# Kernel optimization log

Measured on AMD Instinct MI355X. Metric: run time of the kernel, lower is better.

Reference implementation:

```python
import jax, jax.numpy as jnp
import numpy as np

N_HEADS = 8
N_POINTS = 4
LN_EPS = 1e-5


def _ln(x, g, b):
    m = jnp.mean(x, -1, keepdims=True)
    v = jnp.mean((x - m) ** 2, -1, keepdims=True)
    return (x - m) * jax.lax.rsqrt(v + LN_EPS) * g + b


def _mha(q, k, v, wq, bq, wk, bk, wv, bv, wo, bo):
    B, Lq, C = q.shape
    Dh = C // N_HEADS
    Q = (q @ wq.T + bq).reshape(B, Lq, N_HEADS, Dh)
    K = (k @ wk.T + bk).reshape(B, -1, N_HEADS, Dh)
    V = (v @ wv.T + bv).reshape(B, -1, N_HEADS, Dh)
    s = jnp.einsum('bqhd,bkhd->bhqk', Q, K) * (1.0 / float(np.sqrt(Dh)))
    a = jax.nn.softmax(s, -1)
    o = jnp.einsum('bhqk,bkhd->bqhd', a, V).reshape(B, Lq, C)
    return o @ wo.T + bo


def _ref_points(h, w, L):
    ry = jnp.linspace(0.5, h - 0.5, h) / h
    rx = jnp.linspace(0.5, w - 0.5, w) / w
    gy, gx = jnp.meshgrid(ry, rx, indexing='ij')
    ref = jnp.stack([gx.reshape(-1), gy.reshape(-1)], -1)[None]  # (1, h*w, 2)
    return jnp.broadcast_to(ref[:, :, None, :], (1, h * w, L, 2))


def _deform_core(value, shapes, starts, loc, aw):
    # value: (B, Len_in, H, Dh); loc: (B, Lq, H, L, P, 2); aw: (B, Lq, H, L, P)
    B, _, H, Dh = value.shape
    Lq, P = loc.shape[1], loc.shape[4]
    out = jnp.zeros((B, H, Lq, Dh), value.dtype)
    for l in range(shapes.shape[0]):
        Hl, Wl = int(shapes[l, 0]), int(shapes[l, 1])
        s = int(starts[l])
        v = value[:, s:s + Hl * Wl].transpose(0, 2, 1, 3)  # (B, H, Hl*Wl, Dh)
        # grid_sample(align_corners=False, padding_mode='zeros') pixel coords
        xl = loc[:, :, :, l, :, 0] * Wl - 0.5  # (B, Lq, H, P)
        yl = loc[:, :, :, l, :, 1] * Hl - 0.5
        x0 = jnp.floor(xl); y0 = jnp.floor(yl)
        fx = xl - x0; fy = yl - y0
        x0 = x0.astype(jnp.int32); y0 = y0.astype(jnp.int32)
        acc = jnp.zeros((B, H, Lq, P, Dh), value.dtype)
        for dy, dx in ((0, 0), (0, 1), (1, 0), (1, 1)):
            xi = x0 + dx; yi = y0 + dy
            wgt = (fx if dx else 1.0 - fx) * (fy if dy else 1.0 - fy)
            valid = ((xi >= 0) & (xi < Wl) & (yi >= 0) & (yi < Hl)).astype(value.dtype)
            idx = (jnp.clip(yi, 0, Hl - 1) * Wl + jnp.clip(xi, 0, Wl - 1))
            idx = idx.transpose(0, 2, 1, 3).reshape(B, H, Lq * P)
            g = jnp.take_along_axis(v, idx[..., None], axis=2).reshape(B, H, Lq, P, Dh)
            acc = acc + g * (wgt * valid).transpose(0, 2, 1, 3)[..., None]
        out = out + jnp.einsum('bhqpd,bqhp->bhqd', acc, aw[:, :, :, l])
    return out.transpose(0, 2, 1, 3).reshape(B, Lq, H * Dh)


def reference(tgt, query_pos, src, wq, bq, wk, bk, wv, bv, wo, bo, ln2_g, ln2_b,
              w_off, b_off, w_attn, b_attn, w_val, b_val, w_cout, b_cout,
              ln1_g, ln1_b, w1, b1, w2, b2, ln3_g, ln3_b,
              src_spatial_shapes, level_start_index, h, w):
    shapes = np.asarray(src_spatial_shapes)
    starts = np.asarray(level_start_index)
    h = int(h); w = int(w)
    L = shapes.shape[0]
    B, Lq, C = tgt.shape
    Dh = C // N_HEADS
    # --- self attention (post-LN residual) ---
    q = tgt + query_pos
    t2 = _mha(q, q, tgt, wq, bq, wk, bk, wv, bv, wo, bo)
    t = _ln(tgt + t2, ln2_g, ln2_b)
    # --- MSDeformAttn cross attention ---
    qc = t + query_pos
    value = (src @ w_val.T + b_val).reshape(B, -1, N_HEADS, Dh)
    off = (qc @ w_off.T + b_off).reshape(B, Lq, N_HEADS, L, N_POINTS, 2)
    aw = (qc @ w_attn.T + b_attn).reshape(B, Lq, N_HEADS, L * N_POINTS)
    aw = jax.nn.softmax(aw, -1).reshape(B, Lq, N_HEADS, L, N_POINTS)
    norm = jnp.stack([shapes[:, 1].astype(np.float32), shapes[:, 0].astype(np.float32)], -1)  # (L,2): (W,H)
    rp = _ref_points(h, w, L)  # (1, Lq, L, 2)
    loc = rp[:, :, None, :, None, :] + off / norm[None, None, None, :, None, :]
    samp = _deform_core(value, shapes, starts, loc, aw)
    t2 = samp @ w_cout.T + b_cout
    t = _ln(t + t2, ln1_g, ln1_b)
    # --- FFN ---
    t2 = jax.nn.relu(t @ w1.T + b1) @ w2.T + b2
    t = _ln(t + t2, ln3_g, ln3_b)
    return t


def setup_inputs() -> dict:
    key = jax.random.key(0)
    B, C, L, P, dff = 2, 256, 4, 4, 1024
    h = w = 48
    shapes = np.array([[48, 48], [24, 24], [12, 12], [6, 6]], np.int32)
    starts = np.array([0, 2304, 2880, 3024], np.int32)
    Len_in = 3060
    Lq = h * w
    ks = iter(jax.random.split(key, 40))
    def rn(shape, s=0.02):
        return jax.random.normal(next(ks), shape, jnp.float32) * s
    return dict(
        tgt=rn((B, Lq, C), 1.0), query_pos=rn((B, Lq, C), 1.0), src=rn((B, Len_in, C), 1.0),
        wq=rn((C, C)), bq=rn((C,)), wk=rn((C, C)), bk=rn((C,)), wv=rn((C, C)), bv=rn((C,)),
        wo=rn((C, C)), bo=rn((C,)),
        ln2_g=jnp.ones((C,)), ln2_b=jnp.zeros((C,)),
        w_off=rn((N_HEADS * L * P * 2, C)), b_off=rn((N_HEADS * L * P * 2,)),
        w_attn=rn((N_HEADS * L * P, C)), b_attn=rn((N_HEADS * L * P,)),
        w_val=rn((C, C)), b_val=rn((C,)), w_cout=rn((C, C)), b_cout=rn((C,)),
        ln1_g=jnp.ones((C,)), ln1_b=jnp.zeros((C,)),
        w1=rn((dff, C)), b1=rn((dff,)), w2=rn((C, dff)), b2=rn((C,)),
        ln3_g=jnp.ones((C,)), ln3_b=jnp.zeros((C,)),
        src_spatial_shapes=shapes, level_start_index=starts, h=h, w=w)
```

## Files before the change

kernel.cpp:

```cpp
#include <hip/hip_runtime.h>
#include <hip/hip_bf16.h>
#include <math.h>

typedef __hip_bfloat16 bf16;
typedef __attribute__((ext_vector_type(8))) short short8;
typedef __attribute__((ext_vector_type(4))) short short4v;
typedef __attribute__((ext_vector_type(4))) float f32x4;

static constexpr int B   = 2;
static constexpr int LQ  = 2304;
static constexpr int C   = 256;
static constexpr int NH  = 8;
static constexpr int DH  = 32;
static constexpr int NL  = 4;
static constexpr int NP  = 4;
static constexpr int LEN = 3060;
static constexpr int DFF = 1024;
static constexpr int MQ  = B * LQ;
static constexpr int MV  = B * LEN;
static constexpr int SZ1 = MQ * C;

#define MFMA16(a, b, c) __builtin_amdgcn_mfma_f32_16x16x32_bf16(a, b, c, 0, 0, 0)

__device__ __forceinline__ float ldf(const void* p, size_t i, int bf) {
  return bf ? __bfloat162float(((const bf16*)p)[i]) : ((const float*)p)[i];
}
__device__ __forceinline__ short fl2s(float v) {
  bf16 h = __float2bfloat16(v);
  return *(short*)&h;
}
__device__ __forceinline__ short fl2s_fast(float v) {
  union { float f; unsigned u; } x; x.f = v;
  return (short)((x.u + 0x8000u) >> 16);
}
__device__ __forceinline__ float s2fl(short s) {
  return __bfloat162float(*(bf16*)&s);
}
__device__ __forceinline__ int wire_is_bf16(const unsigned* gprobe) {
  return gprobe[0] == 0x3F803F80u;
}
__device__ __forceinline__ float ldbias(const void* b, int n, int fl) {
  return fl ? s2fl(((const short*)b)[n]) : s2fl(fl2s(((const float*)b)[n]));
}
__device__ __forceinline__ short8 add2bf(short8 a, short8 b) {
  short8 r;
#pragma unroll
  for (int j = 0; j < 8; ++j) r[j] = fl2s(s2fl(a[j]) + s2fl(b[j]));
  return r;
}

struct GemmJob {
  int Xmode;
  const short* Xbf; const void* Xwire; const void* Xwire2;
  const void* Wwire; const void* bwire;
  void* Y;
  int M, N, K, ldY, col0, relu, out_mode, nblk_x;
  float qscale;
};
struct GemmBatch { GemmJob j[4]; int start[5]; int njobs; };

template <int MR>
__global__ __launch_bounds__(256) void gemm_mfma(GemmBatch nb,
                                                 const unsigned* __restrict__ gprobe) {
  constexpr int MT = MR / 64;
  const int fl = wire_is_bf16(gprobe);
  int id = blockIdx.x;
  int jj = 0;
  while (jj + 1 < nb.njobs && id >= nb.start[jj + 1]) ++jj;
  const GemmJob jb = nb.j[jj];
  const int local = id - nb.start[jj];
  const int bx = local % jb.nblk_x;
  const int by = local / jb.nblk_x;
  const int M = jb.M, N = jb.N, K = jb.K;

  __shared__ short Xs[MR][72];
  __shared__ short Ws[64][72];
  const int tid = threadIdx.x;
  const int wave = tid >> 6, lane = tid & 63;
  const int quad = lane >> 4, l16 = lane & 15;
  const int m0 = bx * MR, n0 = by * 64;
  f32x4 acc[MT][4];
#pragma unroll
  for (int mt = 0; mt < MT; ++mt)
#pragma unroll
    for (int nt = 0; nt < 4; ++nt) acc[mt][nt] = f32x4{0.f, 0.f, 0.f, 0.f};

  const int xrow = (MR == 128) ? (tid >> 1) : (tid >> 2);
  const int xcol = (MR == 128) ? ((tid & 1) * 32) : ((tid & 3) * 16);
  constexpr int XU = (MR == 128) ? 4 : 2;
  const int wrow = tid >> 2;
  const int wcol = (tid & 3) * 16;
  int xr = m0 + xrow; if (xr >= M) xr = M - 1;

  const short* xp16 = nullptr; const float* xpf = nullptr;
  const short* tp16 = nullptr; const short* pp16 = nullptr;
  const float* tpf  = nullptr; const float* ppf  = nullptr;
  if (jb.Xmode == 0) {
    xp16 = jb.Xbf + (size_t)xr * K;
  } else if (jb.Xmode == 2) {
    if (fl) xp16 = (const short*)jb.Xwire + (size_t)xr * K;
    else    xpf  = (const float*)jb.Xwire + (size_t)xr * K;
  } else {
    if (fl) { tp16 = (const short*)jb.Xwire + (size_t)xr * K;
              pp16 = (const short*)jb.Xwire2 + (size_t)xr * K; }
    else    { tpf  = (const float*)jb.Xwire + (size_t)xr * K;
              ppf  = (const float*)jb.Xwire2 + (size_t)xr * K; }
  }
  const short* wp16 = (const short*)jb.Wwire;
  const float* wpf  = (const float*)jb.Wwire;
  const size_t wro = (size_t)(n0 + wrow) * K;

  for (int k0 = 0; k0 < K; k0 += 64) {
    if (xp16) {
#pragma unroll
      for (int u = 0; u < XU; ++u)
        *(short8*)&Xs[xrow][xcol + u * 8] = *(const short8*)(xp16 + k0 + xcol + u * 8);
    } else if (xpf) {
#pragma unroll
      for (int u = 0; u < XU; ++u) {
        const float* s = xpf + k0 + xcol + u * 8;
        short8 r;
#pragma unroll
        for (int j = 0; j < 8; ++j) r[j] = fl2s(s[j]);
        *(short8*)&Xs[xrow][xcol + u * 8] = r;
      }
    } else if (tp16) {
#pragma unroll
      for (int u = 0; u < XU; ++u) {
        short8 t8 = *(const short8*)(tp16 + k0 + xcol + u * 8);
        short8 p8 = *(const short8*)(pp16 + k0 + xcol + u * 8);
        *(short8*)&Xs[xrow][xcol + u * 8] = add2bf(t8, p8);
      }
    } else {
#pragma unroll
      for (int u = 0; u < XU; ++u) {
        const float* t = tpf + k0 + xcol + u * 8;
        const float* p = ppf + k0 + xcol + u * 8;
        short8 r;
#pragma unroll
        for (int j = 0; j < 8; ++j) r[j] = fl2s(t[j] + p[j]);
        *(short8*)&Xs[xrow][xcol + u * 8] = r;
      }
    }
    if (fl) {
      const short* wp = wp16 + wro + k0 + wcol;
      *(short8*)&Ws[wrow][wcol]     = *(const short8*)(wp);
      *(short8*)&Ws[wrow][wcol + 8] = *(const short8*)(wp + 8);
    } else {
      const float* wp = wpf + wro + k0 + wcol;
      short8 w0, w1;
#pragma unroll
      for (int j = 0; j < 8; ++j) { w0[j] = fl2s(wp[j]); w1[j] = fl2s(wp[8 + j]); }
      *(short8*)&Ws[wrow][wcol]     = w0;
      *(short8*)&Ws[wrow][wcol + 8] = w1;
    }
    __syncthreads();
#pragma unroll
    for (int kc = 0; kc < 2; ++kc) {
#pragma unroll
      for (int mt = 0; mt < MT; ++mt) {
        short8 a = *(const short8*)&Xs[wave * (16 * MT) + mt * 16 + l16][kc * 32 + quad * 8];
#pragma unroll
        for (int nt = 0; nt < 4; ++nt) {
          short8 b = *(const short8*)&Ws[nt * 16 + l16][kc * 32 + quad * 8];
          acc[mt][nt] = MFMA16(a, b, acc[mt][nt]);
        }
      }
    }
    __syncthreads();
  }

  if (jb.out_mode == 2) {
#pragma unroll
    for (int mt = 0; mt < MT; ++mt) {
      const int mbase = m0 + wave * (16 * MT) + mt * 16 + quad * 4;
      const int b = mbase / LQ;
      const int qb_ = mbase - b * LQ;
#pragma unroll
      for (int nt = 0; nt < 4; ++nt) {
        const int n = n0 + nt * 16 + l16;
        const float bv = ldbias(jb.bwire, n, fl);
        short4v v4;
#pragma unroll
        for (int r = 0; r < 4; ++r) v4[r] = fl2s(acc[mt][nt][r] + bv);
        *(short4v*)((short*)jb.Y + (size_t)(b * 256 + n) * LQ + qb_) = v4;
      }
    }
    return;
  }
#pragma unroll
  for (int mt = 0; mt < MT; ++mt)
#pragma unroll
    for (int nt = 0; nt < 4; ++nt) {
      const int n = n0 + nt * 16 + l16;
      const float bv = ldbias(jb.bwire, n, fl);
#pragma unroll
      for (int r = 0; r < 4; ++r) {
        const int m = m0 + wave * (16 * MT) + mt * 16 + quad * 4 + r;
        if (m < M) {
          float v = (acc[mt][nt][r] + bv) * jb.qscale;
          if (jb.relu) v = fmaxf(v, 0.f);
          if (jb.out_mode == 1)
            ((short*)jb.Y)[(size_t)m * jb.ldY + jb.col0 + n] = fl2s(v);
          else
            ((float*)jb.Y)[(size_t)m * jb.ldY + jb.col0 + n] = v;
        }
      }
    }
}

struct LnGemmArgs {
  const short* X;
  const void* Wwire; const void* bwire;
  const void* R; int Rmode;
  const void* g; const void* be;
  float* Yf32; short* Y16; void* Yfinal;
  const void* pos; short* Yqc;
  int K;
};

__global__ __launch_bounds__(256) void gemm_ln(LnGemmArgs a,
                                               const unsigned* __restrict__ gprobe) {
  const int fl = wire_is_bf16(gprobe);
  const int K = a.K;
  const int NT = K >> 5;

  __shared__ short Xs[2][16][40];
  __shared__ short Ws[2][256][40];
  __shared__ float red[4][16][2];
  __shared__ float minv[16][2];

  const int tid = threadIdx.x;
  const int wave = tid >> 6, lane = tid & 63;
  const int quad = lane >> 4, l16 = lane & 15;
  const int m0 = blockIdx.x * 16;

  f32x4 acc[4];
#pragma unroll
  for (int nt = 0; nt < 4; ++nt) acc[nt] = f32x4{0.f, 0.f, 0.f, 0.f};

  const int xrow = (tid & 63) >> 2, xcol = (tid & 3) * 8;
  const int wr0 = tid >> 2, wc0 = (tid & 3) * 8;
  const short* xpr = a.X + (size_t)(m0 + xrow) * K + xcol;
  const short* wp16 = (const short*)a.Wwire;
  const float* wpf  = (const float*)a.Wwire;

  auto STAGE = [&](int buf, int k0) {
    if (tid < 64)
      *(short8*)&Xs[buf][xrow][xcol] = *(const short8*)(xpr + k0);
#pragma unroll
    for (int u = 0; u < 4; ++u) {
      const int rr = u * 64 + wr0;
      if (fl) {
        *(short8*)&Ws[buf][rr][wc0] = *(const short8*)(wp16 + (size_t)rr * K + k0 + wc0);
      } else {
        const float* wp = wpf + (size_t)rr * K + k0 + wc0;
        short8 w;
#pragma unroll
        for (int j = 0; j < 8; ++j) w[j] = fl2s(wp[j]);
        *(short8*)&Ws[buf][rr][wc0] = w;
      }
    }
  };

  STAGE(0, 0);
  __syncthreads();
  int cur = 0;
  for (int t = 0; t < NT; ++t) {
    if (t + 1 < NT) STAGE(cur ^ 1, (t + 1) << 5);
    short8 av = *(const short8*)&Xs[cur][l16][quad * 8];
#pragma unroll
    for (int nt = 0; nt < 4; ++nt) {
      short8 bv = *(const short8*)&Ws[cur][wave * 64 + nt * 16 + l16][quad * 8];
      acc[nt] = MFMA16(av, bv, acc[nt]);
    }
    __syncthreads();
    cur ^= 1;
  }

  float gc[4], bc[4], bb[4];
#pragma unroll
  for (int nt = 0; nt < 4; ++nt) {
    const int n = wave * 64 + nt * 16 + l16;
    gc[nt] = ldf(a.g, n, fl);
    bc[nt] = ldf(a.be, n, fl);
    bb[nt] = ldbias(a.bwire, n, fl);
  }
#pragma unroll
  for (int r = 0; r < 4; ++r) {
    const int rloc = quad * 4 + r;
    const size_t row = (size_t)(m0 + rloc);
    float s = 0.f, s2 = 0.f;
#pragma unroll
    for (int nt = 0; nt < 4; ++nt) {
      const int n = wave * 64 + nt * 16 + l16;
      const size_t idx = row * C + n;
      const float rv = (a.Rmode == 1) ? ldf(a.R, idx, fl) : ((const float*)a.R)[idx];
      const float v = acc[nt][r] + bb[nt] + rv;
      acc[nt][r] = v;
      s += v;
      s2 += v * v;
    }
#pragma unroll
    for (int off = 8; off > 0; off >>= 1) {
      s  += __shfl_xor(s, off);
      s2 += __shfl_xor(s2, off);
    }
    if (l16 == 0) { red[wave][rloc][0] = s; red[wave][rloc][1] = s2; }
  }
  __syncthreads();
  if (tid < 16) {
    const float s  = red[0][tid][0] + red[1][tid][0] + red[2][tid][0] + red[3][tid][0];
    const float s2 = red[0][tid][1] + red[1][tid][1] + red[2][tid][1] + red[3][tid][1];
    const float mean = s * (1.f / C);
    const float var = fmaxf(s2 * (1.f / C) - mean * mean, 0.f);
    minv[tid][0] = mean;
    minv[tid][1] = rsqrtf(var + 1e-5f);
  }
  __syncthreads();
#pragma unroll
  for (int r = 0; r < 4; ++r) {
    const int rloc = quad * 4 + r;
    const size_t row = (size_t)(m0 + rloc);
    const float mean = minv[rloc][0], inv = minv[rloc][1];
#pragma unroll
    for (int nt = 0; nt < 4; ++nt) {
      const int n = wave * 64 + nt * 16 + l16;
      const size_t idx = row * C + n;
      const float y = (acc[nt][r] - mean) * inv * gc[nt] + bc[nt];
      if (a.Yfinal) {
        if (fl) ((short*)a.Yfinal)[idx] = fl2s(y);
        else    ((float*)a.Yfinal)[idx] = y;
      } else {
        if (a.Yf32) a.Yf32[idx] = y;
        if (a.Y16)  a.Y16[idx] = fl2s(y);
        if (a.Yqc)  a.Yqc[idx] = fl2s(y + ldf(a.pos, idx, fl));
      }
    }
  }
}

__global__ __launch_bounds__(256) void flash_attn(const short* __restrict__ QK,
                                                  const short* __restrict__ Vt,
                                                  short* __restrict__ Op) {
  constexpr int LDQK = 512;
  constexpr int NC = LQ / 64;
  constexpr int NQT = 3;
  const int qb = blockIdx.x;
  const int bh = blockIdx.y;
  const int b = bh >> 3, h = bh & 7;
  const int tid = threadIdx.x;
  const int wave = tid >> 6, lane = tid & 63;
  const int quad = lane >> 4, l16 = lane & 15;

  __shared__ short Ps[4][16][68];
  __shared__ float lsh[256];

  const int q0 = qb * 48;
  const size_t rowb = (size_t)(b * LQ);
  const short* kcol = QK + 256 + h * DH + quad * 8;
  const short* vt0 = Vt + (size_t)(b * 256 + h * 32 + l16) * LQ + quad * 8;
  const short* vt1 = Vt + (size_t)(b * 256 + h * 32 + 16 + l16) * LQ + quad * 8;

  short8 qfrag[NQT];
#pragma unroll
  for (int qt = 0; qt < NQT; ++qt)
    qfrag[qt] = *(const short8*)(QK + (rowb + q0 + qt * 16 + l16) * LDQK + h * DH + quad * 8);

  f32x4 o0[NQT], o1[NQT];
  float lrow[NQT];
#pragma unroll
  for (int qt = 0; qt < NQT; ++qt) {
    o0[qt] = f32x4{0.f, 0.f, 0.f, 0.f};
    o1[qt] = f32x4{0.f, 0.f, 0.f, 0.f};
    lrow[qt] = 0.f;
  }

  short8 kf[4], vf[4];
  {
    const int k0 = wave * 64;
#pragma unroll
    for (int kt = 0; kt < 4; ++kt)
      kf[kt] = *(const short8*)(kcol + (rowb + k0 + kt * 16 + l16) * LDQK);
    vf[0] = *(const short8*)(vt0 + k0);
    vf[1] = *(const short8*)(vt0 + k0 + 32);
    vf[2] = *(const short8*)(vt1 + k0);
    vf[3] = *(const short8*)(vt1 + k0 + 32);
  }

  for (int c = wave; c < NC; c += 4) {
    short8 kn[4], vn[4];
    if (c + 4 < NC) {
      const int k0n = (c + 4) * 64;
#pragma unroll
      for (int kt = 0; kt < 4; ++kt)
        kn[kt] = *(const short8*)(kcol + (rowb + k0n + kt * 16 + l16) * LDQK);
      vn[0] = *(const short8*)(vt0 + k0n);
      vn[1] = *(const short8*)(vt0 + k0n + 32);
      vn[2] = *(const short8*)(vt1 + k0n);
      vn[3] = *(const short8*)(vt1 + k0n + 32);
    }

#pragma unroll
    for (int qt = 0; qt < NQT; ++qt) {
      f32x4 s[4];
#pragma unroll
      for (int kt = 0; kt < 4; ++kt) {
        f32x4 z = {0.f, 0.f, 0.f, 0.f};
        s[kt] = MFMA16(kf[kt], qfrag[qt], z);
      }

      float ps = 0.f;
#pragma unroll
      for (int kt = 0; kt < 4; ++kt)
#pragma unroll
        for (int r = 0; r < 4; ++r) {
          float p = __expf(s[kt][r]);
          s[kt][r] = p;
          ps += p;
        }
      lrow[qt] += ps;

#pragma unroll
      for (int kt = 0; kt < 4; ++kt) {
        short4v pk;
#pragma unroll
        for (int r = 0; r < 4; ++r) pk[r] = fl2s_fast(s[kt][r]);
        *(short4v*)&Ps[wave][l16][kt * 16 + quad * 4] = pk;
      }

#pragma unroll
      for (int half = 0; half < 2; ++half) {
        short4v a0 = *(const short4v*)&Ps[wave][l16][half * 32 + quad * 8];
        short4v a1 = *(const short4v*)&Ps[wave][l16][half * 32 + quad * 8 + 4];
        short8 afrag;
#pragma unroll
        for (int j = 0; j < 4; ++j) { afrag[j] = a0[j]; afrag[4 + j] = a1[j]; }
        o0[qt] = MFMA16(afrag, vf[half], o0[qt]);
        o1[qt] = MFMA16(afrag, vf[2 + half], o1[qt]);
      }
    }

#pragma unroll
    for (int kt = 0; kt < 4; ++kt) { kf[kt] = kn[kt]; vf[kt] = vn[kt]; }
  }

  float* obuf = (float*)&Ps[0][0][0];
  for (int qt = 0; qt < NQT; ++qt) {
    __syncthreads();
    lsh[(wave * 4 + quad) * 16 + l16] = lrow[qt];
#pragma unroll
    for (int r = 0; r < 4; ++r) {
      const int q = quad * 4 + r;
      obuf[(wave * 16 + q) * 32 + l16] = o0[qt][r];
      obuf[(wave * 16 + q) * 32 + 16 + l16] = o1[qt][r];
    }
    __syncthreads();
#pragma unroll
    for (int e = tid; e < 512; e += 256) {
      const int q = e >> 5, d = e & 31;
      float lg = 0.f;
#pragma unroll
      for (int i = 0; i < 16; ++i) lg += lsh[i * 16 + q];
      float ov = 0.f;
#pragma unroll
      for (int w = 0; w < 4; ++w) ov += obuf[(w * 16 + q) * 32 + d];
      Op[(rowb + q0 + qt * 16 + q) * C + h * DH + d] = fl2s_fast(ov / lg);
    }
  }
}

__global__ __launch_bounds__(256) void deform_kern(const short* __restrict__ value,
                                                   const float* __restrict__ oa,
                                                   const int* __restrict__ shapes,
                                                   const int* __restrict__ starts,
                                                   const int* __restrict__ hp,
                                                   const int* __restrict__ wp,
                                                   short* __restrict__ samp) {
  const int bq = blockIdx.x * 4 + (threadIdx.x >> 6);
  const int b = bq / LQ, q = bq % LQ;
  const int lane = threadIdx.x & 63;
  const int h_ = lane >> 3;
  const int d0 = (lane & 7) * 4;

  const int w0 = *wp, h0 = *hp;
  const int qx = q % w0, qy = q / w0;
  const float refx = (qx + 0.5f) / (float)w0;
  const float refy = (qy + 0.5f) / (float)h0;

  const float* offp = oa + (size_t)bq * 384 + h_ * 32;
  const float* awraw = oa + (size_t)bq * 384 + 256 + h_ * 16;

  float e[16];
  float mm = -1e30f;
#pragma unroll
  for (int j = 0; j < 16; ++j) mm = fmaxf(mm, awraw[j]);
  float ssum = 0.f;
#pragma unroll
  for (int j = 0; j < 16; ++j) {
    e[j] = __expf(awraw[j] - mm);
    ssum += e[j];
  }
  const float sinv = 1.f / ssum;

  float acc0 = 0.f, acc1 = 0.f, acc2 = 0.f, acc3 = 0.f;
  for (int l = 0; l < NL; ++l) {
    const int Hl = shapes[l * 2 + 0];
    const int Wl = shapes[l * 2 + 1];
    const int st = starts[l];
    const short* vbase = value + ((size_t)(b * LEN + st)) * C + h_ * DH + d0;
#pragma unroll
    for (int p = 0; p < NP; ++p) {
      const float ox = offp[l * 8 + p * 2 + 0];
      const float oy = offp[l * 8 + p * 2 + 1];
      const float a = e[l * 4 + p] * sinv;
      const float xl = refx * Wl + ox - 0.5f;
      const float yl = refy * Hl + oy - 0.5f;
      const float x0f = floorf(xl), y0f = floorf(yl);
      const float fx = xl - x0f, fy = yl - y0f;
      const int x0 = (int)x0f, y0 = (int)y0f;
#pragma unroll
      for (int corner = 0; corner < 4; ++corner) {
        const int dx = corner & 1, dy = corner >> 1;
        const int xi = x0 + dx, yi = y0 + dy;
        const float wx = dx ? fx : 1.f - fx;
        const float wy = dy ? fy : 1.f - fy;
        const bool valid = (xi >= 0) & (xi < Wl) & (yi >= 0) & (yi < Hl);
        if (valid) {
          const float w = a * wx * wy;
          short4v v4 = *(const short4v*)(vbase + (size_t)(yi * Wl + xi) * C);
          acc0 += w * s2fl(v4[0]);
          acc1 += w * s2fl(v4[1]);
          acc2 += w * s2fl(v4[2]);
          acc3 += w * s2fl(v4[3]);
        }
      }
    }
  }
  short4v out;
  out[0] = fl2s(acc0); out[1] = fl2s(acc1); out[2] = fl2s(acc2); out[3] = fl2s(acc3);
  *(short4v*)(samp + (size_t)bq * C + h_ * DH + d0) = out;
}

extern "C" void kernel_launch(void* const* d_in, const int* in_sizes, int n_in,
                              void* d_out, int out_size, void* d_ws, size_t ws_size,
                              hipStream_t stream) {
  const void* tgt       = d_in[0];
  const void* query_pos = d_in[1];
  const void* src       = d_in[2];
  const void* wq = d_in[3];  const void* bq = d_in[4];
  const void* wk = d_in[5];  const void* bk = d_in[6];
  const void* wv = d_in[7];  const void* bv = d_in[8];
  const void* wo = d_in[9];  const void* bo = d_in[10];
  const void* ln2_g = d_in[11]; const void* ln2_b = d_in[12];
  const void* w_off = d_in[13]; const void* b_off = d_in[14];
  const void* w_attn = d_in[15]; const void* b_attn = d_in[16];
  const void* w_val = d_in[17]; const void* b_val = d_in[18];
  const void* w_cout = d_in[19]; const void* b_cout = d_in[20];
  const void* ln1_g = d_in[21]; const void* ln1_b = d_in[22];
  const void* w1 = d_in[23]; const void* b1 = d_in[24];
  const void* w2 = d_in[25]; const void* b2 = d_in[26];
  const void* ln3_g = d_in[27]; const void* ln3_b = d_in[28];
  const int* shapes = (const int*)d_in[29];
  const int* starts = (const int*)d_in[30];
  const int* hp = (const int*)d_in[31];
  const int* wp = (const int*)d_in[32];
  const unsigned* gprobe = (const unsigned*)ln2_g;

  short* q16    = (short*)((char*)d_ws + 256);
  short* qk_out = q16 + SZ1;
  short* vt16   = qk_out + (size_t)MQ * 512;
  short* ao16   = vt16 + SZ1;
  short* valb   = ao16 + SZ1;
  short* ffn1   = valb + (size_t)MV * C;
  short* t1_16  = ffn1 + (size_t)MQ * DFF;
  float* t_32   = (float*)(t1_16 + SZ1);
  float* t1_32  = t_32 + SZ1;
  float* oa     = t1_32 + SZ1;

  const float scale = 1.f / sqrtf((float)DH);
  const dim3 blk(256);
  const int NX128 = MQ / 128;
  const int NX64  = MQ / 64;
  const int NX16  = MQ / 16;
  const int NXV   = (MV + 127) / 128;

  {
    GemmBatch nb;
    nb.njobs = 4;
    nb.j[0] = {4, nullptr, tgt, query_pos, wq, bq, qk_out,
               MQ, 256, 256, 512, 0, 0, 1, NX128, scale};
    nb.j[1] = {4, nullptr, tgt, query_pos, wk, bk, qk_out,
               MQ, 256, 256, 512, 256, 0, 1, NX128, 1.f};
    nb.j[2] = {2, nullptr, tgt, nullptr, wv, bv, vt16,
               MQ, 256, 256, 0, 0, 0, 2, NX128, 1.f};
    nb.j[3] = {2, nullptr, src, nullptr, w_val, b_val, valb,
               MV, 256, 256, 256, 0, 0, 1, NXV, 1.f};
    nb.start[0] = 0;
    nb.start[1] = NX128 * 4;
    nb.start[2] = nb.start[1] + NX128 * 4;
    nb.start[3] = nb.start[2] + NX128 * 4;
    nb.start[4] = nb.start[3] + NXV * 4;
    gemm_mfma<128><<<nb.start[4], blk, 0, stream>>>(nb, gprobe);
  }
  flash_attn<<<dim3(LQ / 48, B * NH), blk, 0, stream>>>(qk_out, vt16, ao16);

  {
    LnGemmArgs a;
    a.X = ao16; a.Wwire = wo; a.bwire = bo;
    a.R = tgt; a.Rmode = 1; a.g = ln2_g; a.be = ln2_b;
    a.Yf32 = t_32; a.Y16 = nullptr; a.Yfinal = nullptr;
    a.pos = query_pos; a.Yqc = q16;
    a.K = 256;
    gemm_ln<<<NX16, blk, 0, stream>>>(a, gprobe);
  }

  {
    GemmBatch nb;
    nb.njobs = 2;
    nb.j[0] = {0, q16, nullptr, nullptr, w_off, b_off, oa,
               MQ, 256, 256, 384, 0, 0, 0, NX64, 1.f};
    nb.j[1] = {0, q16, nullptr, nullptr, w_attn, b_attn, oa,
               MQ, 128, 256, 384, 256, 0, 0, NX64, 1.f};
    nb.start[0] = 0;
    nb.start[1] = NX64 * 4;
    nb.start[2] = nb.start[1] + NX64 * 2;
    gemm_mfma<64><<<nb.start[2], blk, 0, stream>>>(nb, gprobe);
  }
  deform_kern<<<MQ / 4, blk, 0, stream>>>(valb, oa, shapes, starts, hp, wp, ao16);

  {
    LnGemmArgs a;
    a.X = ao16; a.Wwire = w_cout; a.bwire = b_cout;
    a.R = t_32; a.Rmode = 2; a.g = ln1_g; a.be = ln1_b;
    a.Yf32 = t1_32; a.Y16 = t1_16; a.Yfinal = nullptr;
    a.pos = nullptr; a.Yqc = nullptr;
    a.K = 256;
    gemm_ln<<<NX16, blk, 0, stream>>>(a, gprobe);
  }

  {
    GemmBatch nb;
    nb.njobs = 1;
    nb.j[0] = {0, t1_16, nullptr, nullptr, w1, b1, ffn1,
               MQ, 1024, 256, 1024, 0, 1, 1, NX128, 1.f};
    nb.start[0] = 0; nb.start[1] = NX128 * 16;
    gemm_mfma<128><<<nb.start[1], blk, 0, stream>>>(nb, gprobe);
  }
  {
    LnGemmArgs a;
    a.X = ffn1; a.Wwire = w2; a.bwire = b2;
    a.R = t1_32; a.Rmode = 2; a.g = ln3_g; a.be = ln3_b;
    a.Yf32 = nullptr; a.Y16 = nullptr; a.Yfinal = d_out;
    a.pos = nullptr; a.Yqc = nullptr;
    a.K = 1024;
    gemm_ln<<<NX16, blk, 0, stream>>>(a, gprobe);
  }
}
```

Baseline: 336.0 us.

## Split fused GEMM+LayerNorm into tiled MFMA GEMM plus separate row LayerNorm kernel

Replaces the gemm_ln kernel, which used 16-row tiles with the whole 256-wide weight staged per block, with the generic 64-row-tiled MFMA GEMM writing fp32 to a new scratch buffer. A standalone LayerNorm kernel then adds the residual, normalizes and writes the same outputs. The aim is better weight reuse and occupancy in the GEMM, since the 16-row tiles reloaded the full weight matrix for every block. In exchange, each of the three LayerNorm sites now runs an extra launch and makes an extra fp32 round trip through global memory.

Result: faster. 284.6 us (-15.3%).

```diff
diff --git a/kernel.cpp b/kernel.cpp
--- a/kernel.cpp
+++ b/kernel.cpp
@@ -209,134 +209,103 @@
     }
 }
 
-struct LnGemmArgs {
-  const short* X;
-  const void* Wwire; const void* bwire;
-  const void* R; int Rmode;
-  const void* g; const void* be;
-  float* Yf32; short* Y16; void* Yfinal;
-  const void* pos; short* Yqc;
-  int K;
-};
-
-__global__ __launch_bounds__(256) void gemm_ln(LnGemmArgs a,
-                                               const unsigned* __restrict__ gprobe) {
+__global__ __launch_bounds__(256) void ln_kern(const void* __restrict__ A, int a_mode,
+                                               const float* __restrict__ R,
+                                               const void* __restrict__ g,
+                                               const void* __restrict__ be,
+                                               float* __restrict__ Yf32,
+                                               short* __restrict__ Y16,
+                                               void* __restrict__ Yfinal,
+                                               const void* __restrict__ pos,
+                                               short* __restrict__ Yqc,
+                                               int rows, const unsigned* __restrict__ gprobe) {
   const int fl = wire_is_bf16(gprobe);
-  const int K = a.K;
-  const int NT = K >> 5;
-
-  __shared__ short Xs[2][16][40];
-  __shared__ short Ws[2][256][40];
-  __shared__ float red[4][16][2];
-  __shared__ float minv[16][2];
-
-  const int tid = threadIdx.x;
-  const int wave = tid >> 6, lane = tid & 63;
-  const int quad = lane >> 4, l16 = lane & 15;
-  const int m0 = blockIdx.x * 16;
-
-  f32x4 acc[4];
-#pragma unroll
-  for (int nt = 0; nt < 4; ++nt) acc[nt] = f32x4{0.f, 0.f, 0.f, 0.f};
-
-  const int xrow = (tid & 63) >> 2, xcol = (tid & 3) * 8;
-  const int wr0 = tid >> 2, wc0 = (tid & 3) * 8;
-  const short* xpr = a.X + (size_t)(m0 + xrow) * K + xcol;
-  const short* wp16 = (const short*)a.Wwire;
-  const float* wpf  = (const float*)a.Wwire;
-
-  auto STAGE = [&](int buf, int k0) {
-    if (tid < 64)
-      *(short8*)&Xs[buf][xrow][xcol] = *(const short8*)(xpr + k0);
-#pragma unroll
-    for (int u = 0; u < 4; ++u) {
-      const int rr = u * 64 + wr0;
-      if (fl) {
-        *(short8*)&Ws[buf][rr][wc0] = *(const short8*)(wp16 + (size_t)rr * K + k0 + wc0);
-      } else {
-        const float* wp = wpf + (size_t)rr * K + k0 + wc0;
-        short8 w;
-#pragma unroll
-        for (int j = 0; j < 8; ++j) w[j] = fl2s(wp[j]);
-        *(short8*)&Ws[buf][rr][wc0] = w;
-      }
-    }
-  };
-
-  STAGE(0, 0);
-  __syncthreads();
-  int cur = 0;
-  for (int t = 0; t < NT; ++t) {
-    if (t + 1 < NT) STAGE(cur ^ 1, (t + 1) << 5);
-    short8 av = *(const short8*)&Xs[cur][l16][quad * 8];
-#pragma unroll
-    for (int nt = 0; nt < 4; ++nt) {
-      short8 bv = *(const short8*)&Ws[cur][wave * 64 + nt * 16 + l16][quad * 8];
-      acc[nt] = MFMA16(av, bv, acc[nt]);
-    }
-    __syncthreads();
-    cur ^= 1;
-  }
-
-  float gc[4], bc[4], bb[4];
-#pragma unroll
-  for (int nt = 0; nt < 4; ++nt) {
-    const int n = wave * 64 + nt * 16 + l16;
-    gc[nt] = ldf(a.g, n, fl);
-    bc[nt] = ldf(a.be, n, fl);
-    bb[nt] = ldbias(a.bwire, n, fl);
-  }
-#pragma unroll
-  for (int r = 0; r < 4; ++r) {
-    const int rloc = quad * 4 + r;
-    const size_t row = (size_t)(m0 + rloc);
-    float s = 0.f, s2 = 0.f;
-#pragma unroll
-    for (int nt = 0; nt < 4; ++nt) {
-      const int n = wave * 64 + nt * 16 + l16;
-      const size_t idx = row * C + n;
-      const float rv = (a.Rmode == 1) ? ldf(a.R, idx, fl) : ((const float*)a.R)[idx];
-      const float v = acc[nt][r] + bb[nt] + rv;
-      acc[nt][r] = v;
-      s += v;
-      s2 += v * v;
-    }
-#pragma unroll
-    for (int off = 8; off > 0; off >>= 1) {
-      s  += __shfl_xor(s, off);
-      s2 += __shfl_xor(s2, off);
-    }
-    if (l16 == 0) { red[wave][rloc][0] = s; red[wave][rloc][1] = s2; }
-  }
-  __syncthreads();
-  if (tid < 16) {
-    const float s  = red[0][tid][0] + red[1][tid][0] + red[2][tid][0] + red[3][tid][0];
-    const float s2 = red[0][tid][1] + red[1][tid][1] + red[2][tid][1] + red[3][tid][1];
-    const float mean = s * (1.f / C);
-    const float var = fmaxf(s2 * (1.f / C) - mean * mean, 0.f);
-    minv[tid][0] = mean;
-    minv[tid][1] = rsqrtf(var + 1e-5f);
-  }
-  __syncthreads();
-#pragma unroll
-  for (int r = 0; r < 4; ++r) {
-    const int rloc = quad * 4 + r;
-    const size_t row = (size_t)(m0 + rloc);
-    const float mean = minv[rloc][0], inv = minv[rloc][1];
-#pragma unroll
-    for (int nt = 0; nt < 4; ++nt) {
-      const int n = wave * 64 + nt * 16 + l16;
-      const size_t idx = row * C + n;
-      const float y = (acc[nt][r] - mean) * inv * gc[nt] + bc[nt];
-      if (a.Yfinal) {
-        if (fl) ((short*)a.Yfinal)[idx] = fl2s(y);
-        else    ((float*)a.Yfinal)[idx] = y;
-      } else {
-        if (a.Yf32) a.Yf32[idx] = y;
-        if (a.Y16)  a.Y16[idx] = fl2s(y);
-        if (a.Yqc)  a.Yqc[idx] = fl2s(y + ldf(a.pos, idx, fl));
-      }
-    }
+  const int row = blockIdx.x * 4 + (threadIdx.x >> 6);
+  const int lane = threadIdx.x & 63;
+  if (row >= rows) return;
+  const int c0 = lane * 4;
+  const size_t base = (size_t)row * C + c0;
+
+  float x[4];
+  if (a_mode == 1 && fl) {
+    short4v a4 = *(const short4v*)((const short*)A + base);
+#pragma unroll
+    for (int j = 0; j < 4; ++j) x[j] = s2fl(a4[j]);
+  } else {
+    f32x4 a4 = *(const f32x4*)((const float*)A + base);
+#pragma unroll
+    for (int j = 0; j < 4; ++j) x[j] = a4[j];
+  }
+  f32x4 r4 = *(const f32x4*)(R + base);
+  float s = 0.f, s2 = 0.f;
+#pragma unroll
+  for (int j = 0; j < 4; ++j) { x[j] += r4[j]; s += x[j]; s2 += x[j] * x[j]; }
+#pragma unroll
+  for (int off = 32; off > 0; off >>= 1) {
+    s += __shfl_xor(s, off);
+    s2 += __shfl_xor(s2, off);
+  }
+  const float mean = s * (1.f / C);
+  const float var = fmaxf(s2 * (1.f / C) - mean * mean, 0.f);
+  const float inv = rsqrtf(var + 1e-5f);
+
+  float gv[4], bvv[4];
+  if (fl) {
+    short4v g4 = *(const short4v*)((const short*)g + c0);
+    short4v b4 = *(const short4v*)((const short*)be + c0);
+#pragma unroll
+    for (int j = 0; j < 4; ++j) { gv[j] = s2fl(g4[j]); bvv[j] = s2fl(b4[j]); }
+  } else {
+    f32x4 g4 = *(const f32x4*)((const float*)g + c0);
+    f32x4 b4 = *(const f32x4*)((const float*)be + c0);
+#pragma unroll
+    for (int j = 0; j < 4; ++j) { gv[j] = g4[j]; bvv[j] = b4[j]; }
+  }
+  float y[4];
+#pragma unroll
+  for (int j = 0; j < 4; ++j) y[j] = (x[j] - mean) * inv * gv[j] + bvv[j];
+
+  if (Yfinal) {
+    if (fl) {
+      short4v o;
+#pragma unroll
+      for (int j = 0; j < 4; ++j) o[j] = fl2s(y[j]);
+      *(short4v*)((short*)Yfinal + base) = o;
+    } else {
+      f32x4 o;
+#pragma unroll
+      for (int j = 0; j < 4; ++j) o[j] = y[j];
+      *(f32x4*)((float*)Yfinal + base) = o;
+    }
+    return;
+  }
+  if (Yf32) {
+    f32x4 o;
+#pragma unroll
+    for (int j = 0; j < 4; ++j) o[j] = y[j];
+    *(f32x4*)(Yf32 + base) = o;
+  }
+  if (Y16) {
+    short4v o;
+#pragma unroll
+    for (int j = 0; j < 4; ++j) o[j] = fl2s(y[j]);
+    *(short4v*)(Y16 + base) = o;
+  }
+  if (Yqc) {
+    float pv[4];
+    if (fl) {
+      short4v p4 = *(const short4v*)((const short*)pos + base);
+#pragma unroll
+      for (int j = 0; j < 4; ++j) pv[j] = s2fl(p4[j]);
+    } else {
+      f32x4 p4 = *(const f32x4*)((const float*)pos + base);
+#pragma unroll
+      for (int j = 0; j < 4; ++j) pv[j] = p4[j];
+    }
+    short4v o;
+#pragma unroll
+    for (int j = 0; j < 4; ++j) o[j] = fl2s(y[j] + pv[j]);
+    *(short4v*)(Yqc + base) = o;
   }
 }
 
@@ -574,7 +543,8 @@
   short* valb   = ao16 + SZ1;
   short* ffn1   = valb + (size_t)MV * C;
   short* t1_16  = ffn1 + (size_t)MQ * DFF;
-  float* t_32   = (float*)(t1_16 + SZ1);
+  float* t2a    = (float*)(t1_16 + SZ1);
+  float* t_32   = t2a + SZ1;
   float* t1_32  = t_32 + SZ1;
   float* oa     = t1_32 + SZ1;
 
@@ -582,7 +552,6 @@
   const dim3 blk(256);
   const int NX128 = MQ / 128;
   const int NX64  = MQ / 64;
-  const int NX16  = MQ / 16;
   const int NXV   = (MV + 127) / 128;
 
   {
@@ -606,14 +575,15 @@
   flash_attn<<<dim3(LQ / 48, B * NH), blk, 0, stream>>>(qk_out, vt16, ao16);
 
   {
-    LnGemmArgs a;
-    a.X = ao16; a.Wwire = wo; a.bwire = bo;
-    a.R = tgt; a.Rmode = 1; a.g = ln2_g; a.be = ln2_b;
-    a.Yf32 = t_32; a.Y16 = nullptr; a.Yfinal = nullptr;
-    a.pos = query_pos; a.Yqc = q16;
-    a.K = 256;
-    gemm_ln<<<NX16, blk, 0, stream>>>(a, gprobe);
-  }
+    GemmBatch nb;
+    nb.njobs = 1;
+    nb.j[0] = {0, ao16, nullptr, nullptr, wo, bo, t2a,
+               MQ, 256, 256, 256, 0, 0, 0, NX64, 1.f};
+    nb.start[0] = 0; nb.start[1] = NX64 * 4;
+    gemm_mfma<64><<<nb.start[1], blk, 0, stream>>>(nb, gprobe);
+  }
+  ln_kern<<<MQ / 4, blk, 0, stream>>>(tgt, 1, t2a, ln2_g, ln2_b,
+                                      t_32, nullptr, nullptr, query_pos, q16, MQ, gprobe);
 
   {
     GemmBatch nb;
@@ -630,14 +600,15 @@
   deform_kern<<<MQ / 4, blk, 0, stream>>>(valb, oa, shapes, starts, hp, wp, ao16);
 
   {
-    LnGemmArgs a;
-    a.X = ao16; a.Wwire = w_cout; a.bwire = b_cout;
-    a.R = t_32; a.Rmode = 2; a.g = ln1_g; a.be = ln1_b;
-    a.Yf32 = t1_32; a.Y16 = t1_16; a.Yfinal = nullptr;
-    a.pos = nullptr; a.Yqc = nullptr;
-    a.K = 256;
-    gemm_ln<<<NX16, blk, 0, stream>>>(a, gprobe);
-  }
+    GemmBatch nb;
+    nb.njobs = 1;
+    nb.j[0] = {0, ao16, nullptr, nullptr, w_cout, b_cout, t2a,
+               MQ, 256, 256, 256, 0, 0, 0, NX64, 1.f};
+    nb.start[0] = 0; nb.start[1] = NX64 * 4;
+    gemm_mfma<64><<<nb.start[1], blk, 0, stream>>>(nb, gprobe);
+  }
+  ln_kern<<<MQ / 4, blk, 0, stream>>>(t_32, 2, t2a, ln1_g, ln1_b,
+                                      t1_32, t1_16, nullptr, nullptr, nullptr, MQ, gprobe);
 
   {
     GemmBatch nb;
@@ -648,12 +619,13 @@
     gemm_mfma<128><<<nb.start[1], blk, 0, stream>>>(nb, gprobe);
   }
   {
-    LnGemmArgs a;
-    a.X = ffn1; a.Wwire = w2; a.bwire = b2;
-    a.R = t1_32; a.Rmode = 2; a.g = ln3_g; a.be = ln3_b;
-    a.Yf32 = nullptr; a.Y16 = nullptr; a.Yfinal = d_out;
-    a.pos = nullptr; a.Yqc = nullptr;
-    a.K = 1024;
-    gemm_ln<<<NX16, blk, 0, stream>>>(a, gprobe);
-  }
-}
+    GemmBatch nb;
+    nb.njobs = 1;
+    nb.j[0] = {0, ffn1, nullptr, nullptr, w2, b2, t2a,
+               MQ, 256, 1024, 256, 0, 0, 0, NX64, 1.f};
+    nb.start[0] = 0; nb.start[1] = NX64 * 4;
+    gemm_mfma<64><<<nb.start[1], blk, 0, stream>>>(nb, gprobe);
+  }
+  ln_kern<<<MQ / 4, blk, 0, stream>>>(t1_32, 2, t2a, ln3_g, ln3_b,
+                                      nullptr, nullptr, d_out, nullptr, nullptr, MQ, gprobe);
+}
```
